# Performance work log

Measured on AMD Instinct MI355X. Metric: run time of the kernel, lower is better.

The kernel has to match this reference:

```python
import jax, jax.numpy as jnp
import numpy as np

N_SEGMENT = 8   # frames per clip (init arg n_segment)
P = 4           # patch_size (init arg)
EPS = 1e-5      # torch F.layer_norm default eps


def setup_inputs() -> dict:
    key = jax.random.key(0)
    # (b*t, c, h, w) = (16*8, 256, 28, 28)
    x = jax.random.normal(key, (128, 256, 28, 28), dtype=jnp.float32)
    return {"x": x}


def _layer_norm(x):
    # F.layer_norm over last dim, no affine params
    m = jnp.mean(x, axis=-1, keepdims=True)
    v = jnp.var(x, axis=-1, keepdims=True)
    return (x - m) * jax.lax.rsqrt(v + EPS)


def _self_attention(x):
    # q = k = v = x; scores = softmax(q k^T / sqrt(E)); out = scores @ v
    e = x.shape[-1]
    scores = jnp.einsum('bqe,bke->bqk', x, x) * (1.0 / float(np.sqrt(e)))
    scores = jax.nn.softmax(scores, axis=-1)
    return jnp.einsum('bqk,bke->bqe', scores, x)


def reference(x):
    t, p = N_SEGMENT, P
    bt, c, h, w = x.shape
    b = bt // t
    ph, pw = h // p, w // p
    e = p * p * c  # patch embedding dim = 4096

    # rearrange '(b t) c (ph p1) (pw p2) -> (b ph pw) t (p1 p2 c)'
    y = x.reshape(b, t, c, ph, p, pw, p)
    y = y.transpose(0, 3, 5, 1, 4, 6, 2).reshape(b * ph * pw, t, e)

    # temporal: layernorm + shift-left-diff + self-attention + residual
    xn = _layer_norm(y)
    xn = jnp.concatenate([xn[:, 1:], jnp.zeros_like(xn[:, :1])], axis=1) - xn
    y = _self_attention(xn) + y

    # rearrange '(b ph pw) t e -> (b t) (ph pw) e'
    y = y.reshape(b, ph, pw, t, e).transpose(0, 3, 1, 2, 4).reshape(b * t, ph * pw, e)

    # spatial: layernorm + self-attention + residual
    xn = _layer_norm(y)
    y = _self_attention(xn) + y

    # rearrange '(b t) (ph pw) (p1 p2 c) -> (b t) c (ph p1) (pw p2)'
    y = y.reshape(b, t, ph, pw, p, p, c)
    y = y.transpose(0, 1, 6, 2, 4, 3, 5).reshape(bt, c, h, w)
    return y
```

## Files before the change

kernel.cpp:

```cpp
#include <hip/hip_runtime.h>


#define IDX36(a,b) ((((a)*8)+(b))-((((a)*((a)+1)))/2))

typedef __attribute__((ext_vector_type(8)))  short bf16x8;
typedef __attribute__((ext_vector_type(16))) float f32x16;

__device__ __forceinline__ float wsum64(float v){
  #pragma unroll
  for (int off=32; off; off>>=1) v += __shfl_xor(v, off);
  return v;
}
__device__ __forceinline__ float wsum32(float v){
  #pragma unroll
  for (int off=16; off; off>>=1) v += __shfl_xor(v, off);
  return v;
}
__device__ __forceinline__ unsigned int rne_bf16(float f){
  unsigned int b = __float_as_uint(f);
  return (b + 0x7FFFu + ((b>>16)&1u)) >> 16;
}

__global__ __launch_bounds__(256) void k_t1(const float* __restrict__ x, float* __restrict__ wsG){
  const int bx = blockIdx.x;
  const int b = bx / 112;
  const int ph = (bx % 112) / 16;
  const int slice = bx & 15;
  const int c0 = slice * 16;
  const int tid = threadIdx.x;

  __shared__ float lds[8*16*116];
  const float4* x4 = reinterpret_cast<const float4*>(x);

  #pragma unroll
  for (int t=0;t<8;t++){
    const int base = ((b*8+t)*256 + c0)*196 + ph*28;
    {
      const int f = tid, c = f/28, m = f%28;
      *reinterpret_cast<float4*>(&lds[(t*16+c)*116 + m*4]) = x4[base + c*196 + m];
    }
    if (tid < 192){
      const int f = 256+tid, c = f/28, m = f%28;
      *reinterpret_cast<float4*>(&lds[(t*16+c)*116 + m*4]) = x4[base + c*196 + m];
    }
  }
  __syncthreads();

  const int pw   = tid >> 5;
  const int slot = tid & 31;
  const int c    = slot >> 1;
  const int p1b  = (slot & 1) * 2;

  float v[8][8];
  #pragma unroll
  for (int t=0;t<8;t++){
    const float* p = &lds[(t*16+c)*116 + p1b*28 + pw*4];
    const float4 a  = *reinterpret_cast<const float4*>(p);
    const float4 b2 = *reinterpret_cast<const float4*>(p + 28);
    v[t][0]=a.x;  v[t][1]=a.y;  v[t][2]=a.z;  v[t][3]=a.w;
    v[t][4]=b2.x; v[t][5]=b2.y; v[t][6]=b2.z; v[t][7]=b2.w;
  }

  float Au[36], sm[8];
  #pragma unroll
  for (int a2=0;a2<8;a2++){
    float s0 = 0.f;
    #pragma unroll
    for (int e=0;e<8;e++) s0 += v[a2][e];
    sm[a2] = s0;
    #pragma unroll
    for (int b2=a2;b2<8;b2++){
      float s = 0.f;
      #pragma unroll
      for (int e=0;e<8;e++) s += v[a2][e]*v[b2][e];
      Au[IDX36(a2,b2)] = s;
    }
  }
  #pragma unroll
  for (int i=0;i<36;i++) Au[i] = wsum32(Au[i]);
  #pragma unroll
  for (int t=0;t<8;t++) sm[t] = wsum32(sm[t]);

  if (slot == 0 && pw < 7){
    const int base = ((b*49 + ph*7 + pw)*16 + slice)*44;
    #pragma unroll
    for (int i=0;i<36;i++) wsG[base+i] = Au[i];
    #pragma unroll
    for (int t=0;t<8;t++)  wsG[base+36+t] = sm[t];
  }
}

__global__ __launch_bounds__(64) void k_t2(const float* __restrict__ wsG, float* __restrict__ wsWt){
  const int seq = blockIdx.x;
  const int lane = threadIdx.x;
  __shared__ float red[44];
  if (lane < 44){
    float a = 0.f;
    #pragma unroll
    for (int s=0;s<16;s++) a += wsG[(seq*16+s)*44 + lane];
    red[lane] = a;
  }
  __syncthreads();
  if (lane < 8){
    const int i = lane;
    float Ar[36], mean[8], rstd[8];
    #pragma unroll
    for (int k=0;k<36;k++) Ar[k] = red[k];
    #pragma unroll
    for (int t=0;t<8;t++){
      const float sv = red[36+t];
      mean[t] = sv * (1.f/4096.f);
      const float var = Ar[IDX36(t,t)] * (1.f/4096.f) - mean[t]*mean[t];
      rstd[t] = rsqrtf(var + 1e-5f);
    }
    #define GV(a,b) ((((a)<8)&&((b)<8)) ? (rstd[(a)]*rstd[(b)]*(Ar[((a)<=(b))?IDX36((a),(b)):IDX36((b),(a))] - 4096.f*mean[(a)]*mean[(b)])) : 0.f)
    float l[8]; float mx = -1e30f;
    #pragma unroll
    for (int j=0;j<8;j++){
      const float sij = GV(i+1,j+1) - GV(i+1,j) - GV(i,j+1) + GV(i,j);
      l[j] = sij * (1.f/64.f);
      mx = fmaxf(mx, l[j]);
    }
    float ss = 0.f;
    #pragma unroll
    for (int j=0;j<8;j++){ l[j] = __expf(l[j]-mx); ss += l[j]; }
    const float inv = 1.f/ss;
    float cc = 0.f;
    #pragma unroll
    for (int k2=0;k2<8;k2++){
      const float q = (((k2>=1)? l[k2-1] : 0.f) - l[k2]) * inv;
      const float wv2 = q * rstd[k2];
      wsWt[seq*72 + i*8 + k2] = wv2;
      cc -= wv2 * mean[k2];
    }
    wsWt[seq*72 + 64 + i] = cc;
    #undef GV
  }
}

__global__ __launch_bounds__(256) void k_t3(const float* __restrict__ x, const float* __restrict__ wsWt,
                                            float* __restrict__ y1){
  const int bx = blockIdx.x;
  const int b = bx / 112;
  const int ph = (bx % 112) / 16;
  const int slice = bx & 15;
  const int c0 = slice * 16;
  const int tid = threadIdx.x;

  __shared__ float Wl[7][72];
  for (int idx=tid; idx<504; idx+=256)
    Wl[idx/72][idx%72] = wsWt[(b*49 + ph*7 + idx/72)*72 + idx%72];
  __syncthreads();

  const float4* x4 = reinterpret_cast<const float4*>(x);
  float4* y4 = reinterpret_cast<float4*>(y1);

  #pragma unroll
  for (int fi=0; fi<2; fi++){
    const int f = fi*256 + tid;
    if (f < 448){
      const int c = f/28, m = f%28, pw = m%7, p1 = m/7;
      float4 v[8];
      #pragma unroll
      for (int t=0;t<8;t++) v[t] = x4[((b*8+t)*256 + c0+c)*196 + ph*28 + m];
      const float* W = Wl[pw];
      const int pp = ph*7 + pw;
      #pragma unroll
      for (int i=0;i<8;i++){
        const float ci = W[64+i];
        float4 o;
        o.x = v[i].x + ci; o.y = v[i].y + ci; o.z = v[i].z + ci; o.w = v[i].w + ci;
        #pragma unroll
        for (int j=0;j<8;j++){
          const float w = W[i*8+j];
          o.x += w*v[j].x; o.y += w*v[j].y; o.z += w*v[j].z; o.w += w*v[j].w;
        }
        y4[((b*8+i)*49 + pp)*1024 + (c0+c)*4 + p1] = o;
      }
    }
  }
}

__global__ __launch_bounds__(256,2) void k_s1(const float* __restrict__ y1, float* __restrict__ wsA){
  const int bt = blockIdx.x >> 2;
  const int slice = blockIdx.x & 3;
  const int tid = threadIdx.x;
  const int wave = tid >> 6, lane = tid & 63;

  __shared__ unsigned short Ah[64*136];
  __shared__ unsigned short Al[64*136];
  __shared__ float red[64*52];

  for (int i=tid; i<64*52; i+=256) red[i] = 0.f;

  f32x16 acc00, acc01, acc11;
  #pragma unroll
  for (int i=0;i<16;i++){ acc00[i]=0.f; acc01[i]=0.f; acc11[i]=0.f; }

  const float4* yb4 = reinterpret_cast<const float4*>(y1 + bt*49*4096 + slice*1024);
  const int rgrp = tid >> 5;
  const int col4 = tid & 31;
  const int r0 = lane & 31;
  const int koff = (lane >> 5) * 8;

#define ISSUE_CH(pf, ch) { \
  _Pragma("unroll") \
  for (int i=0;i<7;i++) pf[i] = yb4[(i*8 + rgrp)*1024 + (ch)*32 + col4]; }

#define CW_CH(pf) { \
  _Pragma("unroll") \
  for (int i=0;i<8;i++){ \
    unsigned int h01,h23,l01,l23; \
    if (i==7){ h01=0u; h23=0u; l01=0u; l23=0u; } \
    else { \
      const float4 v = pf[i]; \
      const unsigned int u0=__float_as_uint(v.x), u1=__float_as_uint(v.y); \
      const unsigned int u2=__float_as_uint(v.z), u3=__float_as_uint(v.w); \
      const float l0 = v.x-__uint_as_float(u0&0xFFFF0000u); \
      const float l1 = v.y-__uint_as_float(u1&0xFFFF0000u); \
      const float l2 = v.z-__uint_as_float(u2&0xFFFF0000u); \
      const float l3 = v.w-__uint_as_float(u3&0xFFFF0000u); \
      h01 = (u0>>16)|(u1&0xFFFF0000u); h23 = (u2>>16)|(u3&0xFFFF0000u); \
      l01 = rne_bf16(l0)|(rne_bf16(l1)<<16); l23 = rne_bf16(l2)|(rne_bf16(l3)<<16); \
      if (i==6){ \
        const bool valid = (rgrp==0); const bool ones = (rgrp==1); \
        h01 = valid ? h01 : (ones ? 0x3F803F80u : 0u); \
        h23 = valid ? h23 : (ones ? 0x3F803F80u : 0u); \
        l01 = valid ? l01 : 0u; l23 = valid ? l23 : 0u; \
      } \
    } \
    const int wb = (i*8+rgrp)*136 + col4*4; \
    *reinterpret_cast<uint2*>(&Ah[wb]) = make_uint2(h01,h23); \
    *reinterpret_cast<uint2*>(&Al[wb]) = make_uint2(l01,l23); \
  } }

#define MFMA_CH() { \
  _Pragma("unroll") \
  for (int kk=0;kk<2;kk++){ \
    const int kw = (wave + kk*4)*16; \
    const bf16x8 f0h = *reinterpret_cast<const bf16x8*>(&Ah[ r0     *136 + kw + koff]); \
    const bf16x8 f0l = *reinterpret_cast<const bf16x8*>(&Al[ r0     *136 + kw + koff]); \
    const bf16x8 f1h = *reinterpret_cast<const bf16x8*>(&Ah[(32+r0)*136 + kw + koff]); \
    const bf16x8 f1l = *reinterpret_cast<const bf16x8*>(&Al[(32+r0)*136 + kw + koff]); \
    acc00 = __builtin_amdgcn_mfma_f32_32x32x16_bf16(f0h, f0h, acc00, 0,0,0); \
    acc00 = __builtin_amdgcn_mfma_f32_32x32x16_bf16(f0h, f0l, acc00, 0,0,0); \
    acc00 = __builtin_amdgcn_mfma_f32_32x32x16_bf16(f0l, f0h, acc00, 0,0,0); \
    acc01 = __builtin_amdgcn_mfma_f32_32x32x16_bf16(f0h, f1h, acc01, 0,0,0); \
    acc01 = __builtin_amdgcn_mfma_f32_32x32x16_bf16(f0h, f1l, acc01, 0,0,0); \
    acc01 = __builtin_amdgcn_mfma_f32_32x32x16_bf16(f0l, f1h, acc01, 0,0,0); \
    acc11 = __builtin_amdgcn_mfma_f32_32x32x16_bf16(f1h, f1h, acc11, 0,0,0); \
    acc11 = __builtin_amdgcn_mfma_f32_32x32x16_bf16(f1h, f1l, acc11, 0,0,0); \
    acc11 = __builtin_amdgcn_mfma_f32_32x32x16_bf16(f1l, f1h, acc11, 0,0,0); \
  } }

  float4 pfA[7], pfB[7];
  ISSUE_CH(pfA, 0);
  #pragma unroll
  for (int ch=0; ch<8; ch+=2){
    if (ch+1<8) ISSUE_CH(pfB, ch+1);
    __syncthreads();
    CW_CH(pfA);
    __syncthreads();
    MFMA_CH();
    if (ch+2<8) ISSUE_CH(pfA, ch+2);
    __syncthreads();
    CW_CH(pfB);
    __syncthreads();
    MFMA_CH();
  }
  __syncthreads();

  const int ccol = lane & 31;
  const int rbase = 4*(lane>>5);
  #pragma unroll
  for (int q2=0;q2<16;q2++){
    const int rr = (q2&3) + 8*(q2>>2) + rbase;
    atomicAdd(&red[ rr    *52 + ccol     ], acc00[q2]);
    atomicAdd(&red[ rr    *52 + 32 + ccol], acc01[q2]);
    atomicAdd(&red[(rr+32)*52 + 32 + ccol], acc11[q2]);
  }
  __syncthreads();
  float* wp = wsA + blockIdx.x * 2500;
  for (int idx=tid; idx<2500; idx+=256){
    const int i2 = idx/50, j2 = idx%50;
    wp[idx] = (i2>=32 && j2<32) ? red[j2*52+i2] : red[i2*52+j2];
  }
#undef ISSUE_CH
#undef CW_CH
#undef MFMA_CH
}

__global__ __launch_bounds__(256) void k_s2(const float* __restrict__ wsA, float* __restrict__ wsWT, float* __restrict__ wsC){
  const int bt = blockIdx.x;
  const int tid = threadIdx.x;
  __shared__ float A[2500];
  __shared__ float m[49], r[49];
  for (int idx=tid; idx<2548; idx+=256) wsWT[bt*2548+idx] = 0.f;
  for (int idx=tid; idx<2500; idx+=256){
    float v = 0.f;
    #pragma unroll
    for (int sl=0; sl<4; sl++) v += wsA[(bt*4+sl)*2500 + idx];
    A[idx] = v;
  }
  __syncthreads();
  if (tid < 49){
    const float mm = A[49*50+tid] * (1.f/4096.f);
    const float var = A[tid*50+tid] * (1.f/4096.f) - mm*mm;
    m[tid]=mm; r[tid]=rsqrtf(var+1e-5f);
  }
  __syncthreads();
  const int wv = tid>>6, lane = tid&63;
  for (int i=wv; i<49; i+=4){
    const float ri = r[i], mi = m[i];
    float rv=0.f, mv=0.f, L=-1e30f;
    if (lane < 49){
      rv = r[lane]; mv = m[lane];
      L = ri*rv*(A[i*50+lane] - 4096.f*mi*mv) * (1.f/64.f);
    }
    float mx = L;
    #pragma unroll
    for (int off=32; off; off>>=1) mx = fmaxf(mx, __shfl_xor(mx, off));
    const float p = (lane<49) ? __expf(L-mx) : 0.f;
    const float ss = wsum64(p);
    const float Wv = (p/ss)*rv;
    if (lane < 49) wsWT[bt*2548 + lane*52 + i] = Wv + ((lane==i) ? 1.f : 0.f);
    const float cp = wsum64(-Wv*mv);
    if (lane == 0) wsC[bt*49+i] = cp;
  }
}

__global__ __launch_bounds__(256,2) void k_s3(const float* __restrict__ y1, const float* __restrict__ wsWT,
                                              const float* __restrict__ wsC, float* __restrict__ out){
  const int bt = blockIdx.x >> 2;
  const int chunk = blockIdx.x & 3;
  const int tid = threadIdx.x;
  __shared__ float WT[49*52];
  __shared__ float cl[49];
  for (int idx=tid; idx<2548; idx+=256) WT[idx] = wsWT[bt*2548+idx];
  if (tid < 49) cl[tid] = wsC[bt*49+tid];
  __syncthreads();

  const int e0 = chunk*1024 + tid*4;
  float4 acc[49];
  #pragma unroll
  for (int i=0;i<49;i++){ acc[i].x=0.f; acc[i].y=0.f; acc[i].z=0.f; acc[i].w=0.f; }
  const float* yb = y1 + bt*49*4096;

  for (int j=0;j<49;++j){
    const float4 v = *reinterpret_cast<const float4*>(yb + j*4096 + e0);
    const float4* wr = reinterpret_cast<const float4*>(&WT[j*52]);
    #pragma unroll
    for (int g=0; g<12; g++){
      const float4 w = wr[g];
      acc[g*4+0].x += w.x*v.x; acc[g*4+0].y += w.x*v.y; acc[g*4+0].z += w.x*v.z; acc[g*4+0].w += w.x*v.w;
      acc[g*4+1].x += w.y*v.x; acc[g*4+1].y += w.y*v.y; acc[g*4+1].z += w.y*v.z; acc[g*4+1].w += w.y*v.w;
      acc[g*4+2].x += w.z*v.x; acc[g*4+2].y += w.z*v.y; acc[g*4+2].z += w.z*v.z; acc[g*4+2].w += w.z*v.w;
      acc[g*4+3].x += w.w*v.x; acc[g*4+3].y += w.w*v.y; acc[g*4+3].z += w.w*v.z; acc[g*4+3].w += w.w*v.w;
    }
    const float w48 = WT[j*52+48];
    acc[48].x += w48*v.x; acc[48].y += w48*v.y; acc[48].z += w48*v.z; acc[48].w += w48*v.w;
  }

  const int c  = e0 >> 4;
  const int p1 = (e0 >> 2) & 3;
  float* ob = out + bt*200704 + c*784 + p1*28;
  #pragma unroll
  for (int i=0;i<49;i++){
    const float ci = cl[i];
    float4 o;
    o.x = acc[i].x + ci; o.y = acc[i].y + ci; o.z = acc[i].z + ci; o.w = acc[i].w + ci;
    *reinterpret_cast<float4*>(ob + (i/7)*112 + (i%7)*4) = o;
  }
}

extern "C" void kernel_launch(void* const* d_in, const int* in_sizes, int n_in,
                              void* d_out, int out_size, void* d_ws, size_t ws_size,
                              hipStream_t stream) {
  const float* x = (const float*)d_in[0];
  float* out = (float*)d_out;
  float* ws  = (float*)d_ws;
  float* y1   = ws;
  float* wsA  = y1 + 25690112;
  float* wsWT = wsA + 512*2500;
  float* wsC  = wsWT + 128*2548;
  float* wsG  = wsA;
  float* wsWt = wsA + 551936;
  hipLaunchKernelGGL(k_t1, dim3(1792), dim3(256), 0, stream, x, wsG);
  hipLaunchKernelGGL(k_t2, dim3(784),  dim3(64),  0, stream, wsG, wsWt);
  hipLaunchKernelGGL(k_t3, dim3(1792), dim3(256), 0, stream, x, wsWt, y1);
  hipLaunchKernelGGL(k_s1, dim3(512),  dim3(256), 0, stream, y1, wsA);
  hipLaunchKernelGGL(k_s2, dim3(128),  dim3(256), 0, stream, wsA, wsWT, wsC);
  hipLaunchKernelGGL(k_s3, dim3(512),  dim3(256), 0, stream, y1, wsWT, wsC, out);
}
```

Measured before the change: 218.4 us.

## Use split-bf16 MFMA for spatial output GEMM in k_s3

Replaces the scalar FP32 FMA loop in the final spatial-attention output kernel with 32x32x16 bf16 MFMA instructions. Both the weight matrix and the y1 tiles are split into high and low bf16 parts, and three products are accumulated (hi*hi, hi*lo, lo*hi) to approximate fp32 accuracy. The bias is folded in as an extra K column of ones. Y tiles are staged through LDS per wave, with register prefetch of the next tile. This removes heavy VALU work and large register pressure, but costs extra LDS traffic and scattered scalar stores to the output, and accuracy is slightly below full fp32.

```diff
diff --git a/kernel.cpp b/kernel.cpp
--- a/kernel.cpp
+++ b/kernel.cpp
@@ -334,43 +334,118 @@
   const int bt = blockIdx.x >> 2;
   const int chunk = blockIdx.x & 3;
   const int tid = threadIdx.x;
-  __shared__ float WT[49*52];
-  __shared__ float cl[49];
-  for (int idx=tid; idx<2548; idx+=256) WT[idx] = wsWT[bt*2548+idx];
-  if (tid < 49) cl[tid] = wsC[bt*49+tid];
-  __syncthreads();
-
-  const int e0 = chunk*1024 + tid*4;
-  float4 acc[49];
-  #pragma unroll
-  for (int i=0;i<49;i++){ acc[i].x=0.f; acc[i].y=0.f; acc[i].z=0.f; acc[i].w=0.f; }
-  const float* yb = y1 + bt*49*4096;
-
-  for (int j=0;j<49;++j){
-    const float4 v = *reinterpret_cast<const float4*>(yb + j*4096 + e0);
-    const float4* wr = reinterpret_cast<const float4*>(&WT[j*52]);
-    #pragma unroll
-    for (int g=0; g<12; g++){
-      const float4 w = wr[g];
-      acc[g*4+0].x += w.x*v.x; acc[g*4+0].y += w.x*v.y; acc[g*4+0].z += w.x*v.z; acc[g*4+0].w += w.x*v.w;
-      acc[g*4+1].x += w.y*v.x; acc[g*4+1].y += w.y*v.y; acc[g*4+1].z += w.y*v.z; acc[g*4+1].w += w.y*v.w;
-      acc[g*4+2].x += w.z*v.x; acc[g*4+2].y += w.z*v.y; acc[g*4+2].z += w.z*v.z; acc[g*4+2].w += w.z*v.w;
-      acc[g*4+3].x += w.w*v.x; acc[g*4+3].y += w.w*v.y; acc[g*4+3].z += w.w*v.z; acc[g*4+3].w += w.w*v.w;
-    }
-    const float w48 = WT[j*52+48];
-    acc[48].x += w48*v.x; acc[48].y += w48*v.y; acc[48].z += w48*v.z; acc[48].w += w48*v.w;
-  }
-
-  const int c  = e0 >> 4;
-  const int p1 = (e0 >> 2) & 3;
-  float* ob = out + bt*200704 + c*784 + p1*28;
-  #pragma unroll
-  for (int i=0;i<49;i++){
-    const float ci = cl[i];
-    float4 o;
-    o.x = acc[i].x + ci; o.y = acc[i].y + ci; o.z = acc[i].z + ci; o.w = acc[i].w + ci;
-    *reinterpret_cast<float4*>(ob + (i/7)*112 + (i%7)*4) = o;
-  }
+  const int wave = tid >> 6, lane = tid & 63;
+
+  __shared__ unsigned short Wh[64*68], Wlo[64*68];
+  __shared__ unsigned short Yh[4][32*68], Ylo[4][32*68];
+
+  for (int idx=tid; idx<64*64; idx+=256){
+    const int i = idx>>6, j = idx&63;
+    float v = 0.f;
+    if (i < 49){
+      if (j < 49)       v = wsWT[bt*2548 + j*52 + i];
+      else if (j == 49) v = wsC[bt*49 + i];
+    }
+    const unsigned int u = __float_as_uint(v);
+    const float lo = v - __uint_as_float(u & 0xFFFF0000u);
+    Wh [i*68+j] = (unsigned short)(u>>16);
+    Wlo[i*68+j] = (unsigned short)rne_bf16(lo);
+  }
+  unsigned short* yh = &Yh[wave][0];
+  unsigned short* yl = &Ylo[wave][0];
+  for (int idx=lane; idx<32*16; idx+=64){
+    const int e = idx>>4, jj = idx&15;
+    if (jj > 0){
+      yh[e*68 + 48 + jj] = (jj==1) ? 0x3F80 : 0;
+      yl[e*68 + 48 + jj] = 0;
+    }
+  }
+  __syncthreads();
+
+  const int r0 = lane & 31;
+  const int koff = (lane >> 5) * 8;
+  bf16x8 A0h[4], A0l[4], A1h[4], A1l[4];
+  #pragma unroll
+  for (int kk=0;kk<4;kk++){
+    const int off = kk*16 + koff;
+    A0h[kk] = *reinterpret_cast<const bf16x8*>(&Wh [ r0     *68 + off]);
+    A0l[kk] = *reinterpret_cast<const bf16x8*>(&Wlo[ r0     *68 + off]);
+    A1h[kk] = *reinterpret_cast<const bf16x8*>(&Wh [(32+r0)*68 + off]);
+    A1l[kk] = *reinterpret_cast<const bf16x8*>(&Wlo[(32+r0)*68 + off]);
+  }
+
+  const float4* yb4 = reinterpret_cast<const float4*>(y1 + bt*200704 + chunk*1024);
+  float* ob_base = out + bt*200704;
+
+#define S3_LOAD(pf, t) { \
+  _Pragma("unroll") \
+  for (int p=0;p<7;p++){ \
+    const int idx = p*64 + lane; const int j = idx>>3, e4 = idx&7; \
+    pf[p] = make_float4(0.f,0.f,0.f,0.f); \
+    if (j < 49) pf[p] = yb4[j*1024 + ((t)*4+wave)*8 + e4]; \
+  } }
+
+#define S3_WRITE(pf) { \
+  _Pragma("unroll") \
+  for (int p=0;p<7;p++){ \
+    const int idx = p*64 + lane; const int j = idx>>3, e4 = idx&7; \
+    if (j < 49){ \
+      const float vv[4] = {pf[p].x, pf[p].y, pf[p].z, pf[p].w}; \
+      _Pragma("unroll") \
+      for (int s=0;s<4;s++){ \
+        const unsigned int u = __float_as_uint(vv[s]); \
+        const float lo = vv[s] - __uint_as_float(u & 0xFFFF0000u); \
+        yh[(e4*4+s)*68 + j] = (unsigned short)(u>>16); \
+        yl[(e4*4+s)*68 + j] = (unsigned short)rne_bf16(lo); \
+      } \
+    } \
+  } }
+
+  float4 pf[7];
+  S3_LOAD(pf, 0);
+  S3_WRITE(pf);
+
+  #pragma unroll
+  for (int t=0;t<8;t++){
+    if (t < 7) S3_LOAD(pf, t+1);
+
+    f32x16 acc0, acc1;
+    #pragma unroll
+    for (int i=0;i<16;i++){ acc0[i]=0.f; acc1[i]=0.f; }
+
+    #pragma unroll
+    for (int kk=0;kk<4;kk++){
+      const int off = kk*16 + koff;
+      const bf16x8 Bh = *reinterpret_cast<const bf16x8*>(&yh[r0*68 + off]);
+      const bf16x8 Bl = *reinterpret_cast<const bf16x8*>(&yl[r0*68 + off]);
+      acc0 = __builtin_amdgcn_mfma_f32_32x32x16_bf16(A0h[kk], Bh, acc0, 0,0,0);
+      acc0 = __builtin_amdgcn_mfma_f32_32x32x16_bf16(A0h[kk], Bl, acc0, 0,0,0);
+      acc0 = __builtin_amdgcn_mfma_f32_32x32x16_bf16(A0l[kk], Bh, acc0, 0,0,0);
+      acc1 = __builtin_amdgcn_mfma_f32_32x32x16_bf16(A1h[kk], Bh, acc1, 0,0,0);
+      acc1 = __builtin_amdgcn_mfma_f32_32x32x16_bf16(A1h[kk], Bl, acc1, 0,0,0);
+      acc1 = __builtin_amdgcn_mfma_f32_32x32x16_bf16(A1l[kk], Bh, acc1, 0,0,0);
+    }
+
+    {
+      const int ecol = chunk*1024 + (t*4+wave)*32 + r0;
+      const int c  = ecol >> 4;
+      const int p1 = (ecol >> 2) & 3;
+      const int p2 = ecol & 3;
+      float* ob = ob_base + c*784 + p1*28 + p2;
+      const int rbase = 4*(lane>>5);
+      #pragma unroll
+      for (int q=0;q<16;q++){
+        const int i0 = (q&3) + 8*(q>>2) + rbase;
+        ob[(i0/7)*112 + (i0%7)*4] = acc0[q];
+        const int i1 = 32 + i0;
+        if (i1 < 49) ob[(i1/7)*112 + (i1%7)*4] = acc1[q];
+      }
+    }
+
+    if (t < 7) S3_WRITE(pf);
+  }
+#undef S3_LOAD
+#undef S3_WRITE
 }
 
 extern "C" void kernel_launch(void* const* d_in, const int* in_sizes, int n_in,
```

After: 197.7 us. -9.5%, faster.
